# Kernel tuning notes

Hardware: AMD Instinct MI355X
Metric: run time of the kernel (lower is better)

## Reference

```python
import jax, jax.numpy as jnp
import numpy as np

N_QUBITS = 12          # log2(input_num)
DIM = 1 << N_QUBITS    # 4096
BATCH = 4096
OUTPUT_NUM = 10


def setup_inputs() -> dict:
    key = jax.random.key(0)
    k1, k2 = jax.random.split(key)
    x = jax.random.normal(k1, (BATCH, DIM), dtype=jnp.float32)
    # normalized statevectors (amplitude encoding), as a VQC expects
    x = x / jnp.linalg.norm(x, axis=1, keepdims=True)
    theta = jax.random.normal(k2, (2 * N_QUBITS,), dtype=jnp.float32) * jnp.pi
    return {"x": x, "theta": theta}


def _ry(theta):
    # [[cos(t/2), -sin(t/2)], [sin(t/2), cos(t/2)]]
    c, s = jnp.cos(theta / 2), jnp.sin(theta / 2)
    return jnp.stack([jnp.stack([c, -s]), jnp.stack([s, c])]).astype(jnp.complex64)


def _apply_1q(state, U, q, n):
    # state: [2^n, B]; qubit q is bit q of the row index (qubit 0 = LSB,
    # matching the kron ordering temp = kron(gate_i, temp) in the original).
    B = state.shape[1]
    hi = 1 << (n - 1 - q)
    lo = 1 << q
    s = state.reshape(hi, 2, lo * B)
    s = jnp.einsum('ab,xby->xay', U, s)
    return s.reshape(1 << n, B)


def _cz_phase(n):
    # vqc_10 applies CZ on adjacent pairs (n-2-i, n-1-i) for i in 0..n-2,
    # then CZ(0, n-1). CZ is diagonal; the swap sandwiches cancel exactly.
    idx = jnp.arange(1 << n)
    pairs = [(i, i + 1) for i in range(n - 1)] + [(0, n - 1)]
    par = jnp.zeros_like(idx)
    for p, q in pairs:
        par = par + ((idx >> p) & 1) * ((idx >> q) & 1)
    return jnp.where(par % 2 == 1, -1.0, 1.0).astype(jnp.complex64)


def reference(x, theta):
    n = N_QUBITS
    state = x.T.astype(jnp.complex64)            # [2^n, B]
    # first RY layer, thetas[0:n], theta[i] on qubit i
    for q in range(n):
        state = _apply_1q(state, _ry(theta[q]), q, n)
    # CZ entangling layer (diagonal)
    state = state * _cz_phase(n)[:, None]
    # second RY layer, thetas[n:2n]
    for q in range(n):
        state = _apply_1q(state, _ry(theta[n + q]), q, n)
    # measurement: P(qubit k == 1) for the first OUTPUT_NUM qubits
    probs = state.real ** 2 + state.imag ** 2    # [2^n, B]
    idx = jnp.arange(DIM)
    bits = ((idx[:, None] >> jnp.arange(OUTPUT_NUM)[None, :]) & 1).astype(probs.dtype)  # [2^n, K]
    out = jnp.einsum('db,dk->bk', probs, bits)   # [B, OUTPUT_NUM]
    return out
```

## Files before the change

### kernel.cpp

```cpp
#include <hip/hip_runtime.h>
#include <math.h>

#define DIM  4096
#define KOUT 10
#define BATCH 4096

__device__ __forceinline__ int swzAddr(int lin) {
    return lin ^ (((lin >> 6) & 7) << 2);
}

__device__ __forceinline__ float rlane(float v, int lane) {
    return __int_as_float(__builtin_amdgcn_readlane(__float_as_int(v), lane));
}

__device__ __forceinline__ void ldsFence() {
    __builtin_amdgcn_sched_barrier(0);
    asm volatile("s_waitcnt lgkmcnt(0)" ::: "memory");
    __builtin_amdgcn_sched_barrier(0);
}

template<int K>
__device__ __forceinline__ void liftLayer(float r[64], float t, float s) {
#pragma unroll
    for (int m = 0; m < 32; ++m) {
        const int i0 = ((m >> K) << (K + 1)) | (m & ((1 << K) - 1));
        const int i1 = i0 | (1 << K);
        float a = r[i0], b = r[i1];
        float a1 = fmaf(-t, b, a);
        float b1 = fmaf(s, a1, b);
        r[i1] = b1;
        r[i0] = fmaf(-t, b1, a1);
    }
}

__device__ __forceinline__ void transpose64(float r[64], float* lds, int l) {
    float tmp[32];
    ldsFence();
    if (l < 32) {
#pragma unroll
        for (int e4 = 0; e4 < 16; ++e4)
            *reinterpret_cast<float4*>(&lds[swzAddr(l * 64 + e4 * 4)]) =
                make_float4(r[e4 * 4 + 0], r[e4 * 4 + 1],
                            r[e4 * 4 + 2], r[e4 * 4 + 3]);
    }
#pragma unroll
    for (int j = 0; j < 32; ++j)
        tmp[j] = lds[swzAddr(j * 64 + l)];
    ldsFence();
    if (l >= 32) {
#pragma unroll
        for (int e4 = 0; e4 < 16; ++e4)
            *reinterpret_cast<float4*>(&lds[swzAddr((l - 32) * 64 + e4 * 4)]) =
                make_float4(r[e4 * 4 + 0], r[e4 * 4 + 1],
                            r[e4 * 4 + 2], r[e4 * 4 + 3]);
    }
#pragma unroll
    for (int j = 0; j < 32; ++j)
        r[32 + j] = lds[swzAddr(j * 64 + l)];
#pragma unroll
    for (int j = 0; j < 32; ++j)
        r[j] = tmp[j];
}

__global__ __launch_bounds__(64) void vqc_kernel(
        const float* __restrict__ x,
        const float* __restrict__ theta,
        float* __restrict__ out)
{
    __shared__ __align__(16) float lds[2048];
    const int l = threadIdx.x;
    const int b = blockIdx.x;

    float th = theta[l < 24 ? l : 0];
    float qh = 0.25f * th;
    float sq = sinf(qh), cq = cosf(qh);
    float sfull = 2.f * sq * cq;
    float tt, ss;
    if (fabsf(sq) <= fabsf(cq)) { tt = sq / cq;  ss = sfull;  }
    else                        { tt = -cq / sq; ss = -sfull; }

    float r[64];
    const float4* x4 = reinterpret_cast<const float4*>(x + (size_t)b * DIM + l * 64);
#pragma unroll
    for (int e4 = 0; e4 < 16; ++e4) {
        const float4 w = x4[e4];
        r[e4 * 4 + 0] = w.x; r[e4 * 4 + 1] = w.y;
        r[e4 * 4 + 2] = w.z; r[e4 * 4 + 3] = w.w;
    }

    liftLayer<0>(r, rlane(tt, 0), rlane(ss, 0));
    liftLayer<1>(r, rlane(tt, 1), rlane(ss, 1));
    liftLayer<2>(r, rlane(tt, 2), rlane(ss, 2));
    liftLayer<3>(r, rlane(tt, 3), rlane(ss, 3));
    liftLayer<4>(r, rlane(tt, 4), rlane(ss, 4));
    liftLayer<5>(r, rlane(tt, 5), rlane(ss, 5));

    transpose64(r, lds, l);

    liftLayer<0>(r, rlane(tt, 6),  rlane(ss, 6));
    liftLayer<1>(r, rlane(tt, 7),  rlane(ss, 7));
    liftLayer<2>(r, rlane(tt, 8),  rlane(ss, 8));
    liftLayer<3>(r, rlane(tt, 9),  rlane(ss, 9));
    liftLayer<4>(r, rlane(tt, 10), rlane(ss, 10));
    liftLayer<5>(r, rlane(tt, 11), rlane(ss, 11));

    {
        int f  = __popc(l & (l >> 1) & 0x1F) & 1;
        int l5 = (l >> 5) & 1, l0 = l & 1;
        float sg0 = f              ? -1.f : 1.f;
        float sg1 = (f ^ l5)       ? -1.f : 1.f;
        float sg2 = (f ^ l0)       ? -1.f : 1.f;
        float sg3 = (f ^ l5 ^ l0)  ? -1.f : 1.f;
#pragma unroll
        for (int e = 0; e < 64; ++e) {
            const int Ce  = __popc(e & (e >> 1) & 0x1F) & 1;
            const int sel = (e & 1) | (((e >> 5) & 1) << 1);
            float sgn;
            if      (sel == 0) sgn = sg0;
            else if (sel == 1) sgn = sg1;
            else if (sel == 2) sgn = sg2;
            else               sgn = sg3;
            r[e] *= (Ce ? -sgn : sgn);
        }
    }

    liftLayer<0>(r, rlane(tt, 18), rlane(ss, 18));
    liftLayer<1>(r, rlane(tt, 19), rlane(ss, 19));
    liftLayer<2>(r, rlane(tt, 20), rlane(ss, 20));
    liftLayer<3>(r, rlane(tt, 21), rlane(ss, 21));
    liftLayer<4>(r, rlane(tt, 22), rlane(ss, 22));
    liftLayer<5>(r, rlane(tt, 23), rlane(ss, 23));

    transpose64(r, lds, l);

    liftLayer<0>(r, rlane(tt, 12), rlane(ss, 12));
    liftLayer<1>(r, rlane(tt, 13), rlane(ss, 13));
    liftLayer<2>(r, rlane(tt, 14), rlane(ss, 14));
    liftLayer<3>(r, rlane(tt, 15), rlane(ss, 15));
    liftLayer<4>(r, rlane(tt, 16), rlane(ss, 16));
    liftLayer<5>(r, rlane(tt, 17), rlane(ss, 17));

    float psum = 0.f;
#pragma unroll
    for (int j = 0; j < 64; ++j) psum = fmaf(r[j], r[j], psum);

    float v[10];
#pragma unroll
    for (int k = 0; k < 6; ++k) {
        float mk = 0.f;
#pragma unroll
        for (int j = 0; j < 64; ++j)
            if (j & (1 << k)) mk = fmaf(r[j], r[j], mk);
        v[k] = mk;
    }
    v[6] = (l & 1) ? psum : 0.f;
    v[7] = (l & 2) ? psum : 0.f;
    v[8] = (l & 4) ? psum : 0.f;
    v[9] = (l & 8) ? psum : 0.f;

#pragma unroll
    for (int k = 0; k < 10; ++k) {
        float t = v[k];
#pragma unroll
        for (int off = 32; off >= 1; off >>= 1)
            t += __shfl_xor(t, off, 64);
        v[k] = t;
    }

    if (l == 0) {
#pragma unroll
        for (int k = 0; k < KOUT; ++k) out[b * KOUT + k] = v[k];
    }
}

extern "C" void kernel_launch(void* const* d_in, const int* in_sizes, int n_in,
                              void* d_out, int out_size, void* d_ws, size_t ws_size,
                              hipStream_t stream) {
    const float* x     = (const float*)d_in[0];
    const float* theta = (const float*)d_in[1];
    float* out         = (float*)d_out;
    vqc_kernel<<<BATCH, 64, 0, stream>>>(x, theta, out);
}
```

Baseline: 29.12 us.

## Pack four batch rows per block and compute bit-marginals with a tree reduction

Each block now runs four wavefronts, one batch row each, with a private 2048-float LDS slice per wave. Launch bounds change to 256 threads with a min-blocks hint, which aims at more resident waves per CU and fewer tiny blocks to schedule. The per-bit probability sums now come from a pairwise tree (square once, then fold halves) instead of six masked passes over the 64 registers, cutting the FMA count. Packing waves per block adds LDS use per block, and the launch bound may cap registers for the 64-float state.

```diff
diff --git a/kernel.cpp b/kernel.cpp
--- a/kernel.cpp
+++ b/kernel.cpp
@@ -4,6 +4,7 @@
 #define DIM  4096
 #define KOUT 10
 #define BATCH 4096
+#define WPB  4
 
 __device__ __forceinline__ int swzAddr(int lin) {
     return lin ^ (((lin >> 6) & 7) << 2);
@@ -62,14 +63,17 @@
         r[j] = tmp[j];
 }
 
-__global__ __launch_bounds__(64) void vqc_kernel(
+__global__ __launch_bounds__(256, 4) void vqc_kernel(
         const float* __restrict__ x,
         const float* __restrict__ theta,
         float* __restrict__ out)
 {
-    __shared__ __align__(16) float lds[2048];
-    const int l = threadIdx.x;
-    const int b = blockIdx.x;
+    __shared__ __align__(16) float ldsAll[WPB * 2048];
+    const int tid = threadIdx.x;
+    const int l   = tid & 63;
+    const int wid = tid >> 6;
+    const int b   = blockIdx.x * WPB + wid;
+    float* lds = ldsAll + wid * 2048;
 
     float th = theta[l < 24 ? l : 0];
     float qh = 0.25f * th;
@@ -140,19 +144,29 @@
     liftLayer<4>(r, rlane(tt, 16), rlane(ss, 16));
     liftLayer<5>(r, rlane(tt, 17), rlane(ss, 17));
 
-    float psum = 0.f;
+    float v0 = 0.f, v1 = 0.f, v2 = 0.f, v3 = 0.f, v4 = 0.f;
 #pragma unroll
-    for (int j = 0; j < 64; ++j) psum = fmaf(r[j], r[j], psum);
+    for (int j = 0; j < 64; ++j) r[j] = r[j] * r[j];
+    float q32[32];
+#pragma unroll
+    for (int m = 0; m < 32; ++m) { v0 += r[2*m+1]; q32[m] = r[2*m] + r[2*m+1]; }
+    float q16[16];
+#pragma unroll
+    for (int m = 0; m < 16; ++m) { v1 += q32[2*m+1]; q16[m] = q32[2*m] + q32[2*m+1]; }
+    float q8[8];
+#pragma unroll
+    for (int m = 0; m < 8; ++m)  { v2 += q16[2*m+1]; q8[m] = q16[2*m] + q16[2*m+1]; }
+    float q4[4];
+#pragma unroll
+    for (int m = 0; m < 4; ++m)  { v3 += q8[2*m+1]; q4[m] = q8[2*m] + q8[2*m+1]; }
+    float q2[2];
+#pragma unroll
+    for (int m = 0; m < 2; ++m)  { v4 += q4[2*m+1]; q2[m] = q4[2*m] + q4[2*m+1]; }
+    const float v5   = q2[1];
+    const float psum = q2[0] + q2[1];
 
     float v[10];
-#pragma unroll
-    for (int k = 0; k < 6; ++k) {
-        float mk = 0.f;
-#pragma unroll
-        for (int j = 0; j < 64; ++j)
-            if (j & (1 << k)) mk = fmaf(r[j], r[j], mk);
-        v[k] = mk;
-    }
+    v[0] = v0; v[1] = v1; v[2] = v2; v[3] = v3; v[4] = v4; v[5] = v5;
     v[6] = (l & 1) ? psum : 0.f;
     v[7] = (l & 2) ? psum : 0.f;
     v[8] = (l & 4) ? psum : 0.f;
@@ -179,5 +193,5 @@
     const float* x     = (const float*)d_in[0];
     const float* theta = (const float*)d_in[1];
     float* out         = (float*)d_out;
-    vqc_kernel<<<BATCH, 64, 0, stream>>>(x, theta, out);
+    vqc_kernel<<<BATCH / WPB, 256, 0, stream>>>(x, theta, out);
 }
```

After: 31.70 us. +8.9%, slower.
